# Kernel optimization log

Hardware: AMD Instinct MI355X
Metric: run time of the kernel (lower is better)

Reference implementation:

```python
import jax, jax.numpy as jnp
import numpy as np

BATCH, NODES, FEAT, OUT, EIG = 32, 20000, 64, 64, 16

def setup_inputs() -> dict:
    key = jax.random.key(0)
    k1, k2, k3 = jax.random.split(key, 3)
    x = jax.random.normal(k1, (BATCH, NODES, FEAT), dtype=jnp.float32)
    V = jax.random.normal(k2, (NODES, EIG), dtype=jnp.float32)
    # G packs the ParameterList: G[j, i] == self.G[j*num_features + i]
    # (full EIG x EIG matrices; xavier_uniform_ overwrites the diag init)
    G = jax.random.normal(k3, (OUT, FEAT, EIG, EIG), dtype=jnp.float32) * 0.2
    return {"x": x, "V": V, "G": G}

def reference(x, V, G):
    # original: out[b, n, j] = sum_i (V @ G[j,i] @ V.T @ x[b,:,i]) [n]
    # z[b, i, f] = sum_m V[m, f] * x[b, m, i]        (project onto eigenbasis)
    z = jnp.einsum('mf,bmi->bif', V, x)
    # w[b, j, e] = sum_{i, f} G[j, i, e, f] * z[b, i, f]  (spectral filter mix)
    w = jnp.einsum('jief,bif->bje', G, z)
    # out[b, n, j] = sum_e V[n, e] * w[b, j, e]      (back to node space)
    out = jnp.einsum('ne,bje->bnj', V, w)
    return out
```

## Files before the change

### kernel.cpp

```cpp
#include <hip/hip_runtime.h>

#define BATCH 32
#define NODES 20000
#define FEAT  64
#define OUT   64
#define EIG   16

#define NPC   256
#define CHUNKS 79

__global__ void k_zero(float* __restrict__ p, int n) {
    int idx = blockIdx.x * blockDim.x + threadIdx.x;
    if (idx < n) p[idx] = 0.0f;
}

__global__ void k_stage1(const float* __restrict__ x, const float* __restrict__ V,
                         float* __restrict__ z) {
    const int b = blockIdx.y;
    const int n0 = blockIdx.x * NPC;
    const int t = threadIdx.x;

    __shared__ float Vs[NPC * EIG];
    __shared__ float4 red4[64][EIG];

    {
        float4* vd = (float4*)Vs;
        const float4* vsrc = (const float4*)(V + (size_t)n0 * EIG);
        int avail = NODES - n0; if (avail > NPC) avail = NPC;
        const int avail4 = avail * EIG / 4;
#pragma unroll
        for (int k = t; k < NPC * EIG / 4; k += 256)
            vd[k] = (k < avail4) ? vsrc[k] : make_float4(0.f, 0.f, 0.f, 0.f);
    }
    __syncthreads();

    const int ig = t & 15;
    const int ms = t >> 4;

    float4 acc[EIG];
#pragma unroll
    for (int f = 0; f < EIG; f++) acc[f] = make_float4(0.f, 0.f, 0.f, 0.f);

    const float* xb = x + (size_t)b * NODES * FEAT;

#pragma unroll
    for (int j = 0; j < NPC / 16; j++) {
        const int k = j * 16 + ms;
        if (n0 + k < NODES) {
            const float4 xv = *(const float4*)(xb + (size_t)(n0 + k) * FEAT + ig * 4);
            const float4* vr = (const float4*)(Vs + k * EIG);
            const float4 v0 = vr[0], v1 = vr[1], v2 = vr[2], v3 = vr[3];
            const float vf[EIG] = {v0.x,v0.y,v0.z,v0.w, v1.x,v1.y,v1.z,v1.w,
                                   v2.x,v2.y,v2.z,v2.w, v3.x,v3.y,v3.z,v3.w};
#pragma unroll
            for (int f = 0; f < EIG; f++) {
                acc[f].x += xv.x * vf[f];
                acc[f].y += xv.y * vf[f];
                acc[f].z += xv.z * vf[f];
                acc[f].w += xv.w * vf[f];
            }
        }
    }

#pragma unroll
    for (int f = 0; f < EIG; f++) {
        acc[f].x += __shfl_down(acc[f].x, 16); acc[f].x += __shfl_down(acc[f].x, 32);
        acc[f].y += __shfl_down(acc[f].y, 16); acc[f].y += __shfl_down(acc[f].y, 32);
        acc[f].z += __shfl_down(acc[f].z, 16); acc[f].z += __shfl_down(acc[f].z, 32);
        acc[f].w += __shfl_down(acc[f].w, 16); acc[f].w += __shfl_down(acc[f].w, 32);
    }

    const int wv = t >> 6;
    const int l  = t & 63;
    if (l < 16) {
#pragma unroll
        for (int f = 0; f < EIG; f++) red4[wv * 16 + l][f] = acc[f];
    }
    __syncthreads();

    const float* red = (const float*)red4;
    float* zb = z + (size_t)b * FEAT * EIG;
#pragma unroll
    for (int c2 = 0; c2 < 4; c2++) {
        const int p = t * 4 + c2;
        const int i = p >> 4, f = p & 15;
        const int igg = i >> 2, c = i & 3;
        float s = 0.f;
#pragma unroll
        for (int w = 0; w < 4; w++)
            s += red[((w * 16 + igg) * EIG + f) * 4 + c];
        atomicAdd(&zb[p], s);
    }
}

__global__ void k_stage2(const float* __restrict__ G, const float* __restrict__ z,
                         float* __restrict__ w) {
    const int j = blockIdx.x;
    const int b = blockIdx.y;
    const int t = threadIdx.x;

    __shared__ float zs[FEAT * EIG];
    {
        const float4* zsrc = (const float4*)(z + (size_t)b * FEAT * EIG);
        float4* zdst = (float4*)zs;
#pragma unroll
        for (int k = t; k < FEAT * EIG / 4; k += 64) zdst[k] = zsrc[k];
    }
    __syncthreads();

    const int e = t & 15;
    const int s = t >> 4;
    float acc = 0.0f;
    const float* Gj = G + (size_t)j * FEAT * EIG * EIG;

    for (int i = s * 16; i < s * 16 + 16; i++) {
        const float4* gp = (const float4*)(Gj + ((size_t)i * EIG + e) * EIG);
        const float4* zp = (const float4*)(zs + i * EIG);
        const float4 g0 = gp[0], g1 = gp[1], g2 = gp[2], g3 = gp[3];
        const float4 z0 = zp[0], z1 = zp[1], z2 = zp[2], z3 = zp[3];
        acc += g0.x * z0.x + g0.y * z0.y + g0.z * z0.z + g0.w * z0.w
             + g1.x * z1.x + g1.y * z1.y + g1.z * z1.z + g1.w * z1.w
             + g2.x * z2.x + g2.y * z2.y + g2.z * z2.z + g2.w * z2.w
             + g3.x * z3.x + g3.y * z3.y + g3.z * z3.z + g3.w * z3.w;
    }

    __shared__ float red[64];
    red[t] = acc;
    __syncthreads();
    if (s == 0)
        w[((size_t)b * OUT + j) * EIG + e] = red[e] + red[16 + e] + red[32 + e] + red[48 + e];
}

__global__ void k_stage3(const float* __restrict__ V, const float* __restrict__ w,
                         float* __restrict__ out) {
    const int b = blockIdx.y;
    const int n0 = blockIdx.x * NPC;
    const int t = threadIdx.x;
    const int j = t & 63;
    const int wv = t >> 6;

    __shared__ float Vs[NPC * EIG];
    {
        float4* vd = (float4*)Vs;
        const float4* vsrc = (const float4*)(V + (size_t)n0 * EIG);
        int avail = NODES - n0; if (avail > NPC) avail = NPC;
        const int avail4 = avail * EIG / 4;
#pragma unroll
        for (int k = t; k < NPC * EIG / 4; k += 256)
            vd[k] = (k < avail4) ? vsrc[k] : make_float4(0.f, 0.f, 0.f, 0.f);
    }

    const float4* wp = (const float4*)(w + ((size_t)b * OUT + j) * EIG);
    const float4 w0 = wp[0], w1 = wp[1], w2 = wp[2], w3 = wp[3];
    __syncthreads();

    float* ob = out + (size_t)b * NODES * OUT;
    const int nEnd = (NODES - n0 < NPC) ? (NODES - n0) : NPC;

    for (int k = wv; k < nEnd; k += 4) {
        const float4* vr = (const float4*)(Vs + k * EIG);
        const float4 v0 = vr[0], v1 = vr[1], v2 = vr[2], v3 = vr[3];
        float r = v0.x * w0.x + v0.y * w0.y + v0.z * w0.z + v0.w * w0.w
                + v1.x * w1.x + v1.y * w1.y + v1.z * w1.z + v1.w * w1.w
                + v2.x * w2.x + v2.y * w2.y + v2.z * w2.z + v2.w * w2.w
                + v3.x * w3.x + v3.y * w3.y + v3.z * w3.z + v3.w * w3.w;
        ob[(size_t)(n0 + k) * OUT + j] = r;
    }
}

extern "C" void kernel_launch(void* const* d_in, const int* in_sizes, int n_in,
                              void* d_out, int out_size, void* d_ws, size_t ws_size,
                              hipStream_t stream) {
    const float* x = (const float*)d_in[0];
    const float* V = (const float*)d_in[1];
    const float* G = (const float*)d_in[2];
    float* out = (float*)d_out;

    float* z = (float*)d_ws;
    float* w = z + (size_t)BATCH * FEAT * EIG;

    const int zn = BATCH * FEAT * EIG;
    k_zero<<<(zn + 255) / 256, 256, 0, stream>>>(z, zn);

    k_stage1<<<dim3(CHUNKS, BATCH), 256, 0, stream>>>(x, V, z);
    k_stage2<<<dim3(OUT, BATCH), 64, 0, stream>>>(G, z, w);
    k_stage3<<<dim3(CHUNKS, BATCH), 256, 0, stream>>>(V, w, out);
}
```

Measured before the change: 349.2 us.

## Restructure projection and back-projection kernels with register tiling and larger node chunks

Stage 1 now gives each wave a contiguous 160-node range. Each thread computes a 4x4 register tile of (feature, eigen) products and reads V directly from global memory, with no shared-memory staging, which cuts register pressure and the shuffle reduction. Stage 3 has each thread compute four output features per node from register-held w and write a float4, giving vectorized stores instead of scalar ones. Both kernels use fewer, larger blocks with launch bounds, so there are fewer atomics and less per-block overhead, at the cost of fewer blocks to hide memory latency.

```diff
diff --git a/kernel.cpp b/kernel.cpp
--- a/kernel.cpp
+++ b/kernel.cpp
@@ -6,91 +6,66 @@
 #define OUT   64
 #define EIG   16
 
-#define NPC   256
-#define CHUNKS 79
+#define CH1     32
+#define S1_NPB  640
+#define S1_NPW  160
 
 __global__ void k_zero(float* __restrict__ p, int n) {
     int idx = blockIdx.x * blockDim.x + threadIdx.x;
     if (idx < n) p[idx] = 0.0f;
 }
 
-__global__ void k_stage1(const float* __restrict__ x, const float* __restrict__ V,
-                         float* __restrict__ z) {
+__global__ __launch_bounds__(256, 4)
+void k_stage1(const float* __restrict__ x, const float* __restrict__ V,
+              float* __restrict__ z) {
+    const int c = blockIdx.x;
     const int b = blockIdx.y;
-    const int n0 = blockIdx.x * NPC;
     const int t = threadIdx.x;
+    const int lane = t & 63;
+    const int wv   = t >> 6;
+    const int ig   = lane & 15;
+    const int fg   = lane >> 4;
 
-    __shared__ float Vs[NPC * EIG];
-    __shared__ float4 red4[64][EIG];
+    float4 a0 = make_float4(0.f,0.f,0.f,0.f), a1 = a0, a2 = a0, a3 = a0;
 
-    {
-        float4* vd = (float4*)Vs;
-        const float4* vsrc = (const float4*)(V + (size_t)n0 * EIG);
-        int avail = NODES - n0; if (avail > NPC) avail = NPC;
-        const int avail4 = avail * EIG / 4;
-#pragma unroll
-        for (int k = t; k < NPC * EIG / 4; k += 256)
-            vd[k] = (k < avail4) ? vsrc[k] : make_float4(0.f, 0.f, 0.f, 0.f);
+    const int wb = c * S1_NPB + wv * S1_NPW;
+    int cnt = NODES - wb;
+    if (cnt > S1_NPW) cnt = S1_NPW;
+
+    const float* xp = x + ((size_t)b * NODES + wb) * FEAT + ig * 4;
+    const float* vp = V + (size_t)wb * EIG + fg * 4;
+
+#pragma unroll 8
+    for (int m = 0; m < cnt; m++) {
+        const float4 xv = *(const float4*)(xp + (size_t)m * FEAT);
+        const float4 vv = *(const float4*)(vp + (size_t)m * EIG);
+        a0.x += vv.x * xv.x; a0.y += vv.y * xv.x; a0.z += vv.z * xv.x; a0.w += vv.w * xv.x;
+        a1.x += vv.x * xv.y; a1.y += vv.y * xv.y; a1.z += vv.z * xv.y; a1.w += vv.w * xv.y;
+        a2.x += vv.x * xv.z; a2.y += vv.y * xv.z; a2.z += vv.z * xv.z; a2.w += vv.w * xv.z;
+        a3.x += vv.x * xv.w; a3.y += vv.y * xv.w; a3.z += vv.z * xv.w; a3.w += vv.w * xv.w;
     }
+
+    __shared__ float4 red[4][256];
+    red[0][t] = a0; red[1][t] = a1; red[2][t] = a2; red[3][t] = a3;
     __syncthreads();
 
-    const int ig = t & 15;
-    const int ms = t >> 4;
+    const int ls = t >> 2;
+    const int q  = t & 3;
+    float4 s  = red[q][ls];
+    const float4 sb = red[q][ 64 + ls];
+    const float4 sc = red[q][128 + ls];
+    const float4 sd = red[q][192 + ls];
+    s.x += sb.x + sc.x + sd.x;
+    s.y += sb.y + sc.y + sd.y;
+    s.z += sb.z + sc.z + sd.z;
+    s.w += sb.w + sc.w + sd.w;
 
-    float4 acc[EIG];
-#pragma unroll
-    for (int f = 0; f < EIG; f++) acc[f] = make_float4(0.f, 0.f, 0.f, 0.f);
-
-    const float* xb = x + (size_t)b * NODES * FEAT;
-
-#pragma unroll
-    for (int j = 0; j < NPC / 16; j++) {
-        const int k = j * 16 + ms;
-        if (n0 + k < NODES) {
-            const float4 xv = *(const float4*)(xb + (size_t)(n0 + k) * FEAT + ig * 4);
-            const float4* vr = (const float4*)(Vs + k * EIG);
-            const float4 v0 = vr[0], v1 = vr[1], v2 = vr[2], v3 = vr[3];
-            const float vf[EIG] = {v0.x,v0.y,v0.z,v0.w, v1.x,v1.y,v1.z,v1.w,
-                                   v2.x,v2.y,v2.z,v2.w, v3.x,v3.y,v3.z,v3.w};
-#pragma unroll
-            for (int f = 0; f < EIG; f++) {
-                acc[f].x += xv.x * vf[f];
-                acc[f].y += xv.y * vf[f];
-                acc[f].z += xv.z * vf[f];
-                acc[f].w += xv.w * vf[f];
-            }
-        }
-    }
-
-#pragma unroll
-    for (int f = 0; f < EIG; f++) {
-        acc[f].x += __shfl_down(acc[f].x, 16); acc[f].x += __shfl_down(acc[f].x, 32);
-        acc[f].y += __shfl_down(acc[f].y, 16); acc[f].y += __shfl_down(acc[f].y, 32);
-        acc[f].z += __shfl_down(acc[f].z, 16); acc[f].z += __shfl_down(acc[f].z, 32);
-        acc[f].w += __shfl_down(acc[f].w, 16); acc[f].w += __shfl_down(acc[f].w, 32);
-    }
-
-    const int wv = t >> 6;
-    const int l  = t & 63;
-    if (l < 16) {
-#pragma unroll
-        for (int f = 0; f < EIG; f++) red4[wv * 16 + l][f] = acc[f];
-    }
-    __syncthreads();
-
-    const float* red = (const float*)red4;
-    float* zb = z + (size_t)b * FEAT * EIG;
-#pragma unroll
-    for (int c2 = 0; c2 < 4; c2++) {
-        const int p = t * 4 + c2;
-        const int i = p >> 4, f = p & 15;
-        const int igg = i >> 2, c = i & 3;
-        float s = 0.f;
-#pragma unroll
-        for (int w = 0; w < 4; w++)
-            s += red[((w * 16 + igg) * EIG + f) * 4 + c];
-        atomicAdd(&zb[p], s);
-    }
+    float* zp = z + (size_t)b * (FEAT * EIG)
+                  + (size_t)(4 * (ls & 15) + q) * EIG + 4 * (ls >> 4);
+    atomicAdd(zp + 0, s.x);
+    atomicAdd(zp + 1, s.y);
+    atomicAdd(zp + 2, s.z);
+    atomicAdd(zp + 3, s.w);
 }
 
 __global__ void k_stage2(const float* __restrict__ G, const float* __restrict__ z,
@@ -131,40 +106,47 @@
         w[((size_t)b * OUT + j) * EIG + e] = red[e] + red[16 + e] + red[32 + e] + red[48 + e];
 }
 
-__global__ void k_stage3(const float* __restrict__ V, const float* __restrict__ w,
-                         float* __restrict__ out) {
+#define DOT16(u) (v0.x*W[u][0].x + v0.y*W[u][0].y + v0.z*W[u][0].z + v0.w*W[u][0].w \
+                + v1.x*W[u][1].x + v1.y*W[u][1].y + v1.z*W[u][1].z + v1.w*W[u][1].w \
+                + v2.x*W[u][2].x + v2.y*W[u][2].y + v2.z*W[u][2].z + v2.w*W[u][2].w \
+                + v3.x*W[u][3].x + v3.y*W[u][3].y + v3.z*W[u][3].z + v3.w*W[u][3].w)
+
+__global__ __launch_bounds__(256, 4)
+void k_stage3(const float* __restrict__ V, const float* __restrict__ w,
+              float* __restrict__ out) {
+    const int c = blockIdx.x;
     const int b = blockIdx.y;
-    const int n0 = blockIdx.x * NPC;
     const int t = threadIdx.x;
-    const int j = t & 63;
-    const int wv = t >> 6;
+    const int jg = t & 15;
+    const int ns = t >> 4;
 
-    __shared__ float Vs[NPC * EIG];
-    {
-        float4* vd = (float4*)Vs;
-        const float4* vsrc = (const float4*)(V + (size_t)n0 * EIG);
-        int avail = NODES - n0; if (avail > NPC) avail = NPC;
-        const int avail4 = avail * EIG / 4;
+    const float* wp = w + ((size_t)b * OUT + 4 * jg) * EIG;
+    float4 W[4][4];
 #pragma unroll
-        for (int k = t; k < NPC * EIG / 4; k += 256)
-            vd[k] = (k < avail4) ? vsrc[k] : make_float4(0.f, 0.f, 0.f, 0.f);
-    }
+    for (int u = 0; u < 4; u++)
+#pragma unroll
+        for (int vr = 0; vr < 4; vr++)
+            W[u][vr] = *(const float4*)(wp + u * EIG + vr * 4);
 
-    const float4* wp = (const float4*)(w + ((size_t)b * OUT + j) * EIG);
-    const float4 w0 = wp[0], w1 = wp[1], w2 = wp[2], w3 = wp[3];
-    __syncthreads();
+    const int nb = c * 640 + ns;
+    float* ob = out + (size_t)b * NODES * OUT + 4 * jg;
 
-    float* ob = out + (size_t)b * NODES * OUT;
-    const int nEnd = (NODES - n0 < NPC) ? (NODES - n0) : NPC;
-
-    for (int k = wv; k < nEnd; k += 4) {
-        const float4* vr = (const float4*)(Vs + k * EIG);
-        const float4 v0 = vr[0], v1 = vr[1], v2 = vr[2], v3 = vr[3];
-        float r = v0.x * w0.x + v0.y * w0.y + v0.z * w0.z + v0.w * w0.w
-                + v1.x * w1.x + v1.y * w1.y + v1.z * w1.z + v1.w * w1.w
-                + v2.x * w2.x + v2.y * w2.y + v2.z * w2.z + v2.w * w2.w
-                + v3.x * w3.x + v3.y * w3.y + v3.z * w3.z + v3.w * w3.w;
-        ob[(size_t)(n0 + k) * OUT + j] = r;
+#pragma unroll 2
+    for (int it = 0; it < 40; it++) {
+        const int n = nb + it * 16;
+        if (n < NODES) {
+            const float* vp = V + (size_t)n * EIG;
+            const float4 v0 = *(const float4*)(vp);
+            const float4 v1 = *(const float4*)(vp + 4);
+            const float4 v2 = *(const float4*)(vp + 8);
+            const float4 v3 = *(const float4*)(vp + 12);
+            float4 o;
+            o.x = DOT16(0);
+            o.y = DOT16(1);
+            o.z = DOT16(2);
+            o.w = DOT16(3);
+            *(float4*)(ob + (size_t)n * OUT) = o;
+        }
     }
 }
 
@@ -182,7 +164,7 @@
     const int zn = BATCH * FEAT * EIG;
     k_zero<<<(zn + 255) / 256, 256, 0, stream>>>(z, zn);
 
-    k_stage1<<<dim3(CHUNKS, BATCH), 256, 0, stream>>>(x, V, z);
+    k_stage1<<<dim3(CH1, BATCH), 256, 0, stream>>>(x, V, z);
     k_stage2<<<dim3(OUT, BATCH), 64, 0, stream>>>(G, z, w);
-    k_stage3<<<dim3(CHUNKS, BATCH), 256, 0, stream>>>(V, w, out);
+    k_stage3<<<dim3(CH1, BATCH), 256, 0, stream>>>(V, w, out);
 }
```

Measured after the change: 413.8 us. 18.5% more time.
